# Optimization experiments

Hardware: AMD Instinct MI355X
Metric: run time of the kernel (lower is better)

## Reference

```python
import jax, jax.numpy as jnp
import numpy as np

D_MODEL = 1024
D_INNER = 1024
N_HEADS = 16
D_HEAD = D_INNER // N_HEADS
B = 2
CUR = 1024
PREV = 1024
LN_EPS = 1e-5


def _rel_shift(x):
    # x: (b, i, j, h) -- faithful to torch: pad along i, flat-reinterpret, drop first row
    b, i, j, h = x.shape
    zp = jnp.zeros((b, 1, j, h), x.dtype)
    xp = jnp.concatenate([zp, x], axis=1).reshape(i + 1, b, j, h)
    return xp[1:].reshape(b, i, j, h)


def setup_inputs() -> dict:
    key = jax.random.key(0)
    ks = jax.random.split(key, 10)
    x = jax.random.normal(ks[0], (B, CUR, D_MODEL), jnp.float32)
    mem = jax.random.normal(ks[1], (B, PREV, D_MODEL), jnp.float32)
    pos_emb = jax.random.normal(ks[2], (CUR + PREV, D_INNER), jnp.float32)
    u = jax.random.normal(ks[3], (N_HEADS, D_HEAD), jnp.float32) * 0.02
    v = jax.random.normal(ks[4], (N_HEADS, D_HEAD), jnp.float32) * 0.02
    # causal mask: query i (current segment) may attend key j if j <= i + PREV
    idx_i = jnp.arange(CUR)[:, None]
    idx_j = jnp.arange(CUR + PREV)[None, :]
    tgt_mask = jnp.broadcast_to((idx_j > idx_i + PREV)[None, :, :, None], (B, CUR, CUR + PREV, 1))
    Wq = jax.random.normal(ks[5], (D_INNER, D_MODEL), jnp.float32) * 0.02
    Wkv = jax.random.normal(ks[6], (2 * D_INNER, D_MODEL), jnp.float32) * 0.02
    Wfc = jax.random.normal(ks[7], (D_MODEL, D_INNER), jnp.float32) * 0.02
    bfc = jnp.zeros((D_MODEL,), jnp.float32)
    gamma = jnp.ones((D_MODEL,), jnp.float32)
    beta = jnp.zeros((D_MODEL,), jnp.float32)
    return {"x": x, "pos_emb": pos_emb, "u": u, "v": v, "mem": mem,
            "tgt_mask": tgt_mask, "Wq": Wq, "Wkv": Wkv, "Wfc": Wfc,
            "bfc": bfc, "gamma": gamma, "beta": beta}


def reference(x, pos_emb, u, v, mem, tgt_mask, Wq, Wkv, Wfc, bfc, gamma, beta):
    b, cur, _ = x.shape
    prev = mem.shape[1]
    tot = cur + prev
    h_telda = jnp.concatenate([mem, x], axis=1)               # (b, tot, d_model)
    q = jnp.einsum('bsm,im->bsi', x, Wq)                      # (b, cur, d_inner)
    kv = jnp.einsum('bsm,im->bsi', h_telda, Wkv)              # (b, tot, 2*d_inner)
    k, vv = kv[..., :D_INNER], kv[..., D_INNER:]
    q = q.reshape(b, cur, N_HEADS, D_HEAD)
    k = k.reshape(b, tot, N_HEADS, D_HEAD)
    vv = vv.reshape(b, tot, N_HEADS, D_HEAD)
    content = jnp.einsum('bihd,bjhd->bijh', q + u, k)
    pos = pos_emb.reshape(tot, N_HEADS, D_HEAD)
    pos_attn = jnp.einsum('bihd,jhd->bijh', q + v, pos)
    attn = content + _rel_shift(pos_attn)
    attn = jnp.where(tgt_mask, -jnp.inf, attn)
    attn = attn / (D_HEAD ** 0.5)
    attn = jax.nn.softmax(attn, axis=1)  # faithful: softmax over query dim as in original
    out = jnp.einsum('bijh,bjhd->bihd', attn, vv).reshape(b, cur, D_INNER)
    y = x + jnp.einsum('bsi,mi->bsm', out, Wfc) + bfc
    mu = jnp.mean(y, axis=-1, keepdims=True)
    var = jnp.mean((y - mu) ** 2, axis=-1, keepdims=True)
    return (y - mu) / jnp.sqrt(var + LN_EPS) * gamma + beta
```

## Files before the change

kernel.cpp:

```cpp
#include <hip/hip_runtime.h>
#include <hip/hip_bf16.h>
#include <stdint.h>

typedef unsigned short u16;
typedef __attribute__((ext_vector_type(8))) __bf16 bf16x8;
typedef __attribute__((ext_vector_type(4))) float f32x4;
typedef __attribute__((ext_vector_type(4))) float float4v;
typedef __attribute__((ext_vector_type(4))) u16  u16x4;

#define DEV __device__ __forceinline__

#define NB   2
#define CUR  1024
#define PREV 1024
#define TOT  2048
#define DM   1024
#define NH   16
#define DH   64

DEV u16 f2b(float f) {
    uint32_t u = __builtin_bit_cast(uint32_t, f);
    uint32_t r = (u + 0x7fffu + ((u >> 16) & 1u)) >> 16;
    return (u16)r;
}
DEV float b2f(u16 u) {
    return __builtin_bit_cast(float, (uint32_t)u << 16);
}

typedef const __attribute__((address_space(1))) void* gptr_t;
typedef __attribute__((address_space(3))) void*       lptr_t;
DEV void async16(const void* g, void* l) {
    __builtin_amdgcn_global_load_lds((gptr_t)g, (lptr_t)l, 16, 0, 0);
}

template<int BM, int BN, int BK, int WM, int WN, int EPI>
__global__ __launch_bounds__(256)
void gemm_bt(const u16* __restrict__ A, const u16* __restrict__ B,
             int M, int N, int K, long sA, long sB, int bzBase,
             void* __restrict__ C0, void* __restrict__ C1,
             const float* __restrict__ F0, const float* __restrict__ F1)
{
    constexpr int WAVES_N = BN / WN;
    constexpr int MI = WM / 16, NI = WN / 16;
    static_assert((BM / WM) * (BN / WN) == 4, "4 waves");
    static_assert(BK == 64, "swizzle assumes 8 chunks/row");
    static_assert((BM * BK) % 2048 == 0 && (BN * BK) % 2048 == 0, "staging");

    __shared__ u16 lA[BM * BK];
    __shared__ u16 lB[BN * BK];

    const int bz = blockIdx.z;
    const int m0 = blockIdx.y * BM, n0 = blockIdx.x * BN;
    const int tid = threadIdx.x, wave = tid >> 6, lane = tid & 63;

    if constexpr (EPI == 3) {
        if (m0 > n0 + BN - 1 + PREV) return;
    }

    const u16* Ab = A + (long)bz * sA;
    const u16* Bb = B + (long)bz * sB;
    const int wm0 = (wave / WAVES_N) * WM, wn0 = (wave % WAVES_N) * WN;
    const int quad = lane >> 4;

    f32x4 acc[MI][NI];
#pragma unroll
    for (int mi = 0; mi < MI; ++mi)
#pragma unroll
        for (int ni = 0; ni < NI; ++ni)
            acc[mi][ni] = f32x4{0.f, 0.f, 0.f, 0.f};

    int Kend = K;
    if constexpr (EPI == 4) {
        int t = n0 + BN + PREV;
        Kend = t < K ? t : K;
    }

    const int srow = tid >> 3;
    const int ksw  = (((tid & 7) ^ ((tid >> 3) & 7)) << 3);

    for (int kt = 0; kt < Kend; kt += BK) {
        __syncthreads();
#pragma unroll
        for (int is = 0; is < (BM * BK) / 2048; ++is) {
            int r = is * 32 + srow;
            async16(Ab + (long)(m0 + r) * K + kt + ksw, &lA[is * 2048 + wave * 512]);
        }
#pragma unroll
        for (int is = 0; is < (BN * BK) / 2048; ++is) {
            int r = is * 32 + srow;
            async16(Bb + (long)(n0 + r) * K + kt + ksw, &lB[is * 2048 + wave * 512]);
        }
        __syncthreads();
#pragma unroll
        for (int ks = 0; ks < BK; ks += 32) {
            bf16x8 af[MI], br[NI];
#pragma unroll
            for (int mi = 0; mi < MI; ++mi)
                af[mi] = *(const bf16x8*)(const void*)
                    &lA[(wm0 + mi * 16 + (lane & 15)) * BK +
                        ((((ks >> 3) + quad) ^ (lane & 7)) << 3)];
#pragma unroll
            for (int ni = 0; ni < NI; ++ni)
                br[ni] = *(const bf16x8*)(const void*)
                    &lB[(wn0 + ni * 16 + (lane & 15)) * BK +
                        ((((ks >> 3) + quad) ^ (lane & 7)) << 3)];
#pragma unroll
            for (int mi = 0; mi < MI; ++mi)
#pragma unroll
                for (int ni = 0; ni < NI; ++ni)
                    acc[mi][ni] = __builtin_amdgcn_mfma_f32_16x16x32_bf16(af[mi], br[ni], acc[mi][ni], 0, 0, 0);
        }
    }

    const int gbz = bzBase + bz;

    if constexpr (EPI == 1) {
        u16* Abuf = (u16*)C0;
        const int b = gbz;
#pragma unroll
        for (int mi = 0; mi < MI; ++mi) {
            const int m = m0 + wm0 + mi * 16 + quad * 4;
            const int h = m >> 6, d = m & 63;
            const float4v uu = *(const float4v*)(F0 + m);
            const float4v vv = *(const float4v*)(F1 + m);
#pragma unroll
            for (int ni = 0; ni < NI; ++ni) {
                const int i = n0 + wn0 + ni * 16 + (lane & 15);
                u16x4 pu, pv;
#pragma unroll
                for (int r = 0; r < 4; ++r) {
                    pu[r] = f2b(acc[mi][ni][r] + uu[r]);
                    pv[r] = f2b(acc[mi][ni][r] + vv[r]);
                }
                *(u16x4*)(Abuf + (((long)(b * NH + h)) * CUR + i) * 128 + d) = pu;
                if (b == 0) {
                    if (i > 0)
                        *(u16x4*)(Abuf + (((long)h) * CUR + (i - 1)) * 128 + 64 + d) = pv;
                    if (i == 1023) {
                        u16x4 z = {};
                        *(u16x4*)(Abuf + (((long)h) * CUR + 1023) * 128 + 64 + d) = z;
                    }
                } else {
                    *(u16x4*)(Abuf + (((long)(NH + h)) * CUR + i) * 128 + 64 + d) = pv;
                }
            }
        }
    } else if constexpr (EPI == 2) {
#pragma unroll
        for (int mi = 0; mi < MI; ++mi) {
            const int m = m0 + wm0 + mi * 16 + quad * 4;
            const bool isV = m >= DM;
            const int h = (m >> 6) & 15, d = m & 63;
#pragma unroll
            for (int ni = 0; ni < NI; ++ni) {
                const int n = n0 + wn0 + ni * 16 + (lane & 15);
                const int b = n >> 11, j = n & 2047;
                u16x4 p;
#pragma unroll
                for (int r = 0; r < 4; ++r) p[r] = f2b(acc[mi][ni][r]);
                if (!isV)
                    *(u16x4*)((u16*)C0 + (((long)(b * NH + h)) * TOT + j) * 128 + d) = p;
                else
                    *(u16x4*)((u16*)C1 + (((long)(b * NH + h)) * TOT + j) * 64 + d) = p;
            }
        }
    } else if constexpr (EPI == 3) {
        u16* Eb = (u16*)C0 + (long)gbz * ((long)CUR * TOT);
        float ps[MI][4];
#pragma unroll
        for (int mi = 0; mi < MI; ++mi)
#pragma unroll
            for (int r = 0; r < 4; ++r) ps[mi][r] = 0.f;
#pragma unroll
        for (int mi = 0; mi < MI; ++mi) {
            const int m = m0 + wm0 + mi * 16 + quad * 4;
#pragma unroll
            for (int ni = 0; ni < NI; ++ni) {
                const int n = n0 + wn0 + ni * 16 + (lane & 15);
                u16x4 p;
#pragma unroll
                for (int r = 0; r < 4; ++r) {
                    float e = (m + r > n + PREV) ? 0.f : __expf(acc[mi][ni][r] * 0.125f);
                    p[r] = f2b(e);
                    ps[mi][r] += e;
                }
                *(u16x4*)(Eb + (long)n * TOT + m) = p;
            }
        }
        float* CS = (float*)C1 + (long)gbz * TOT;
#pragma unroll
        for (int mi = 0; mi < MI; ++mi)
#pragma unroll
            for (int r = 0; r < 4; ++r) {
                float vv = ps[mi][r];
                vv += __shfl_xor(vv, 1);
                vv += __shfl_xor(vv, 2);
                vv += __shfl_xor(vv, 4);
                vv += __shfl_xor(vv, 8);
                if ((lane & 15) == 0)
                    atomicAdd(CS + m0 + wm0 + mi * 16 + quad * 4 + r, vv);
            }
    } else if constexpr (EPI == 4) {
        const int b = gbz >> 4, h = gbz & 15;
        u16* Ob = (u16*)C0 + (long)b * CUR * DM + h * DH;
#pragma unroll
        for (int mi = 0; mi < MI; ++mi) {
            const int m = m0 + wm0 + mi * 16 + quad * 4;
#pragma unroll
            for (int ni = 0; ni < NI; ++ni) {
                const int n = n0 + wn0 + ni * 16 + (lane & 15);
                u16x4 p;
#pragma unroll
                for (int r = 0; r < 4; ++r) p[r] = f2b(acc[mi][ni][r]);
                *(u16x4*)(Ob + (long)n * DM + m) = p;
            }
        }
    } else if constexpr (EPI == 5) {
#pragma unroll
        for (int mi = 0; mi < MI; ++mi) {
            const int m = m0 + wm0 + mi * 16 + quad * 4;
            const float4v bb = *(const float4v*)(F1 + m);
#pragma unroll
            for (int ni = 0; ni < NI; ++ni) {
                const int n = n0 + wn0 + ni * 16 + (lane & 15);
                const float4v xr = *(const float4v*)(F0 + (long)n * DM + m);
                float4v y;
#pragma unroll
                for (int r = 0; r < 4; ++r) y[r] = xr[r] + acc[mi][ni][r] + bb[r];
                *(float4v*)((float*)C0 + (long)n * DM + m) = y;
            }
        }
    }
}

__global__ __launch_bounds__(256)
void cvt_weights(const float* __restrict__ Wq, const float* __restrict__ Wkv,
                 const float* __restrict__ Wfc, u16* __restrict__ Wqb,
                 u16* __restrict__ Wkvb, u16* __restrict__ Wfcb)
{
    int i = blockIdx.x * 256 + threadIdx.x;
    const float* s; u16* d; int off;
    if (i < 262144)      { s = Wq;  d = Wqb;  off = i; }
    else if (i < 786432) { s = Wkv; d = Wkvb; off = i - 262144; }
    else                 { s = Wfc; d = Wfcb; off = i - 786432; }
    float4v f = ((const float4v*)s)[off];
    u16x4 o = {f2b(f[0]), f2b(f[1]), f2b(f[2]), f2b(f[3])};
    ((u16x4*)d)[off] = o;
}

__global__ __launch_bounds__(256)
void pack_H(const float* __restrict__ mem, const float* __restrict__ x, u16* __restrict__ dst)
{
    int i = blockIdx.x * 256 + threadIdx.x;
    int e = i << 2;
    int b = e >> 21, r = e & ((1 << 21) - 1);
    const float* src = (r < (1 << 20)) ? (mem + ((long)b << 20) + r)
                                       : (x + ((long)b << 20) + (r - (1 << 20)));
    float4v f = *(const float4v*)src;
    u16x4 o = {f2b(f[0]), f2b(f[1]), f2b(f[2]), f2b(f[3])};
    ((u16x4*)dst)[i] = o;
}

__global__ __launch_bounds__(256)
void pack_pos(const float* __restrict__ pos, u16* __restrict__ Bbuf)
{
    int i = blockIdx.x * 256 + threadIdx.x;
    int e = i << 2;
    int h = e >> 17, r = e & 131071, j = r >> 6, d = r & 63;
    float4v f = *(const float4v*)(pos + (long)j * DM + h * DH + d);
    u16x4 o = {f2b(f[0]), f2b(f[1]), f2b(f[2]), f2b(f[3])};
    long base = ((long)h * TOT + j) * 128 + 64 + d;
    *(u16x4*)(Bbuf + base) = o;
    *(u16x4*)(Bbuf + base + (long)NH * TOT * 128) = o;
}

__global__ __launch_bounds__(256)
void vprime_kernel(const u16* __restrict__ Vtmp, const float* __restrict__ colsum,
                   u16* __restrict__ Vp, int bzBase)
{
    __shared__ float t[64][65];
    int bz = bzBase + blockIdx.y;
    int j0 = blockIdx.x * 64;
    const u16* src = Vtmp + ((long)bz * TOT + j0) * 64;
    const float* cs = colsum + (long)bz * TOT + j0;
    for (int e = threadIdx.x; e < 4096; e += 256) {
        int jl = e >> 6, d = e & 63;
        t[jl][d] = b2f(src[e]) / cs[jl];
    }
    __syncthreads();
    u16* dst = Vp + (long)bz * DH * TOT + j0;
    for (int e = threadIdx.x; e < 4096; e += 256) {
        int d = e >> 6, jl = e & 63;
        dst[(long)d * TOT + jl] = f2b(t[jl][d]);
    }
}

__global__ __launch_bounds__(256)
void ln_kernel(const float* __restrict__ Y, const float* __restrict__ gamma,
               const float* __restrict__ beta, float* __restrict__ out)
{
    const int row = blockIdx.x;
    const float* y = Y + (long)row * DM;
    float v[4];
    float s = 0.f;
#pragma unroll
    for (int t = 0; t < 4; ++t) { v[t] = y[threadIdx.x + t * 256]; s += v[t]; }
#pragma unroll
    for (int off = 32; off > 0; off >>= 1) s += __shfl_down(s, off);
    __shared__ float r1[4], r2[4];
    int wv = threadIdx.x >> 6, ln = threadIdx.x & 63;
    if (ln == 0) r1[wv] = s;
    __syncthreads();
    float mu = (r1[0] + r1[1] + r1[2] + r1[3]) * (1.f / DM);
    float q = 0.f;
#pragma unroll
    for (int t = 0; t < 4; ++t) { float d = v[t] - mu; q += d * d; }
#pragma unroll
    for (int off = 32; off > 0; off >>= 1) q += __shfl_down(q, off);
    if (ln == 0) r2[wv] = q;
    __syncthreads();
    float var = (r2[0] + r2[1] + r2[2] + r2[3]) * (1.f / DM);
    float inv = rsqrtf(var + 1e-5f);
#pragma unroll
    for (int t = 0; t < 4; ++t) {
        int c = threadIdx.x + t * 256;
        out[(long)row * DM + c] = (v[t] - mu) * inv * gamma[c] + beta[c];
    }
}

extern "C" void kernel_launch(void* const* d_in, const int* in_sizes, int n_in,
                              void* d_out, int out_size, void* d_ws, size_t ws_size,
                              hipStream_t stream)
{
    const float* x     = (const float*)d_in[0];
    const float* pos   = (const float*)d_in[1];
    const float* u     = (const float*)d_in[2];
    const float* vbias = (const float*)d_in[3];
    const float* mem   = (const float*)d_in[4];
    const float* Wq    = (const float*)d_in[6];
    const float* Wkv   = (const float*)d_in[7];
    const float* Wfc   = (const float*)d_in[8];
    const float* bfc   = (const float*)d_in[9];
    const float* gamma = (const float*)d_in[10];
    const float* beta  = (const float*)d_in[11];
    float* out = (float*)d_out;

    char* w = (char*)d_ws;
    auto alloc = [&](size_t bytes) {
        char* p = w;
        w += (bytes + 255) & ~(size_t)255;
        return p;
    };
    u16*   Hb     = (u16*)alloc(4096UL * 1024 * 2);
    u16*   Wqb    = (u16*)alloc(1024UL * 1024 * 2);
    u16*   Wkvb   = (u16*)alloc(2048UL * 1024 * 2);
    u16*   Wfcb   = (u16*)alloc(1024UL * 1024 * 2);
    u16*   Abuf   = (u16*)alloc(32UL * 1024 * 128 * 2);
    u16*   Bbuf   = (u16*)alloc(32UL * 2048 * 128 * 2);
    u16*   Vtmp   = (u16*)alloc(32UL * 2048 * 64 * 2);
    u16*   Vp     = (u16*)alloc(32UL * 64 * 2048 * 2);
    float* colsum = (float*)alloc(32UL * 2048 * 4);
    u16*   Obf    = (u16*)alloc(2048UL * 1024 * 2);
    float* Yf     = (float*)alloc(2048UL * 1024 * 4);
    u16*   Ebuf   = (u16*)alloc(32UL * 1024 * 2048 * 2);

    hipMemsetAsync(colsum, 0, 32UL * 2048 * 4, stream);

    cvt_weights<<<4096, 256, 0, stream>>>(Wq, Wkv, Wfc, Wqb, Wkvb, Wfcb);
    pack_H  <<<4096, 256, 0, stream>>>(mem, x, Hb);
    pack_pos<<<2048, 256, 0, stream>>>(pos, Bbuf);

    gemm_bt<128, 64, 64, 64, 32, 1><<<dim3(16, 8, 2), 256, 0, stream>>>(
        Wqb, Hb + 1024UL * 1024, 1024, 1024, 1024, 0, 2048L * 1024, 0,
        Abuf, nullptr, u, vbias);
    gemm_bt<128, 128, 64, 64, 64, 2><<<dim3(32, 16, 1), 256, 0, stream>>>(
        Wkvb, Hb, 2048, 4096, 1024, 0, 0, 0, Bbuf, Vtmp, nullptr, nullptr);

    gemm_bt<128, 128, 64, 64, 64, 3><<<dim3(8, 16, 32), 256, 0, stream>>>(
        Bbuf, Abuf, 2048, 1024, 128, 2048L * 128, 1024L * 128, 0,
        Ebuf, colsum, nullptr, nullptr);
    vprime_kernel<<<dim3(32, 32), 256, 0, stream>>>(Vtmp, colsum, Vp, 0);
    gemm_bt<64, 64, 64, 32, 32, 4><<<dim3(16, 1, 32), 256, 0, stream>>>(
        Vp, Ebuf, 64, 1024, 2048, 64L * 2048, 1024L * 2048, 0,
        Obf, nullptr, nullptr, nullptr);

    gemm_bt<64, 128, 64, 32, 64, 5><<<dim3(16, 16, 1), 256, 0, stream>>>(
        Wfcb, Obf, 1024, 2048, 1024, 0, 0, 0, Yf, nullptr, x, bfc);
    ln_kernel<<<2048, 256, 0, stream>>>(Yf, gamma, beta, out);
}
```

Before: 185.2 us.

## Fuse score recompute, column normalization and PV into a flash-style attention kernel

Stops writing the full bf16 exp-score matrix to global memory. The column-sum pass now only accumulates exp sums, and vprime emits reciprocal column sums. A new fused kernel recomputes QK scores per 64-key tile, applies the mask, exp and reciprocal-colsum scaling, and multiplies by V through LDS. This removes a large intermediate write and read (32×1024×2048 bf16) at the cost of computing the QK^T product twice. The new kernel also runs with low parallelism (512 blocks) and uses no pipelining between tile loads and MFMA.

```diff
diff --git a/kernel.cpp b/kernel.cpp
--- a/kernel.cpp
+++ b/kernel.cpp
@@ -44,7 +44,6 @@
     constexpr int MI = WM / 16, NI = WN / 16;
     static_assert((BM / WM) * (BN / WN) == 4, "4 waves");
     static_assert(BK == 64, "swizzle assumes 8 chunks/row");
-    static_assert((BM * BK) % 2048 == 0 && (BN * BK) % 2048 == 0, "staging");
 
     __shared__ u16 lA[BM * BK];
     __shared__ u16 lB[BN * BK];
@@ -69,16 +68,10 @@
         for (int ni = 0; ni < NI; ++ni)
             acc[mi][ni] = f32x4{0.f, 0.f, 0.f, 0.f};
 
-    int Kend = K;
-    if constexpr (EPI == 4) {
-        int t = n0 + BN + PREV;
-        Kend = t < K ? t : K;
-    }
-
     const int srow = tid >> 3;
     const int ksw  = (((tid & 7) ^ ((tid >> 3) & 7)) << 3);
 
-    for (int kt = 0; kt < Kend; kt += BK) {
+    for (int kt = 0; kt < K; kt += BK) {
         __syncthreads();
 #pragma unroll
         for (int is = 0; is < (BM * BK) / 2048; ++is) {
@@ -165,7 +158,6 @@
             }
         }
     } else if constexpr (EPI == 3) {
-        u16* Eb = (u16*)C0 + (long)gbz * ((long)CUR * TOT);
         float ps[MI][4];
 #pragma unroll
         for (int mi = 0; mi < MI; ++mi)
@@ -177,14 +169,11 @@
 #pragma unroll
             for (int ni = 0; ni < NI; ++ni) {
                 const int n = n0 + wn0 + ni * 16 + (lane & 15);
-                u16x4 p;
 #pragma unroll
                 for (int r = 0; r < 4; ++r) {
                     float e = (m + r > n + PREV) ? 0.f : __expf(acc[mi][ni][r] * 0.125f);
-                    p[r] = f2b(e);
                     ps[mi][r] += e;
                 }
-                *(u16x4*)(Eb + (long)n * TOT + m) = p;
             }
         }
         float* CS = (float*)C1 + (long)gbz * TOT;
@@ -200,21 +189,6 @@
                 if ((lane & 15) == 0)
                     atomicAdd(CS + m0 + wm0 + mi * 16 + quad * 4 + r, vv);
             }
-    } else if constexpr (EPI == 4) {
-        const int b = gbz >> 4, h = gbz & 15;
-        u16* Ob = (u16*)C0 + (long)b * CUR * DM + h * DH;
-#pragma unroll
-        for (int mi = 0; mi < MI; ++mi) {
-            const int m = m0 + wm0 + mi * 16 + quad * 4;
-#pragma unroll
-            for (int ni = 0; ni < NI; ++ni) {
-                const int n = n0 + wn0 + ni * 16 + (lane & 15);
-                u16x4 p;
-#pragma unroll
-                for (int r = 0; r < 4; ++r) p[r] = f2b(acc[mi][ni][r]);
-                *(u16x4*)(Ob + (long)n * DM + m) = p;
-            }
-        }
     } else if constexpr (EPI == 5) {
 #pragma unroll
         for (int mi = 0; mi < MI; ++mi) {
@@ -230,6 +204,120 @@
                 *(float4v*)((float*)C0 + (long)n * DM + m) = y;
             }
         }
+    }
+}
+
+__global__ __launch_bounds__(256)
+void fused_attn(const u16* __restrict__ Abuf, const u16* __restrict__ Bbuf,
+                const u16* __restrict__ Vp, const float* __restrict__ rcs,
+                u16* __restrict__ Obf)
+{
+    __shared__ u16 lQ[64 * 128];
+    __shared__ u16 lK[64 * 128];
+    __shared__ u16 lV[64 * 64];
+    __shared__ u16 lP[64 * 64];
+
+    const int bh = blockIdx.y;
+    const int n0 = blockIdx.x * 64;
+    const int b = bh >> 4, h = bh & 15;
+    const int tid = threadIdx.x, wave = tid >> 6, lane = tid & 63;
+    const int l15 = lane & 15, quad = lane >> 4;
+    const int iw = wave * 16 + l15;
+
+    const u16*  Qg = Abuf + ((long)bh * CUR + n0) * 128;
+    const u16*  Kg = Bbuf + (long)bh * TOT * 128;
+    const u16*  Vg = Vp + (long)bh * DH * TOT;
+    const float* rc = rcs + (long)bh * TOT;
+
+    {
+        const int r = tid >> 4, c = tid & 15;
+        const int cs = (c & 8) | ((c & 7) ^ (r & 7));
+#pragma unroll
+        for (int is = 0; is < 4; ++is)
+            async16(Qg + (long)(is * 16 + r) * 128 + cs * 8, &lQ[is * 2048 + wave * 512]);
+    }
+
+    f32x4 oacc[4];
+#pragma unroll
+    for (int mi = 0; mi < 4; ++mi) oacc[mi] = f32x4{0.f, 0.f, 0.f, 0.f};
+
+    const int ig = n0 + iw;
+    const int nt = (n0 >> 6) + 17;
+
+    for (int t = 0; t < nt; ++t) {
+        const int j0 = t * 64;
+        __syncthreads();
+        {
+            const int r = tid >> 4, c = tid & 15;
+            const int cs = (c & 8) | ((c & 7) ^ (r & 7));
+#pragma unroll
+            for (int is = 0; is < 4; ++is)
+                async16(Kg + (long)(j0 + is * 16 + r) * 128 + cs * 8, &lK[is * 2048 + wave * 512]);
+        }
+        {
+            const int r = tid >> 3, c = tid & 7;
+            const int cs = c ^ (r & 7);
+#pragma unroll
+            for (int is = 0; is < 2; ++is)
+                async16(Vg + (long)(is * 32 + r) * TOT + j0 + cs * 8, &lV[is * 2048 + wave * 512]);
+        }
+        __syncthreads();
+
+        f32x4 sacc[4];
+#pragma unroll
+        for (int smi = 0; smi < 4; ++smi) sacc[smi] = f32x4{0.f, 0.f, 0.f, 0.f};
+#pragma unroll
+        for (int ks = 0; ks < 128; ks += 32) {
+            const int cq = (ks >> 3) + quad;
+            const bf16x8 qf = *(const bf16x8*)(const void*)
+                &lQ[iw * 128 + (((cq & 8) | ((cq & 7) ^ (iw & 7))) << 3)];
+#pragma unroll
+            for (int smi = 0; smi < 4; ++smi) {
+                const int jr = smi * 16 + l15;
+                const bf16x8 kf = *(const bf16x8*)(const void*)
+                    &lK[jr * 128 + (((cq & 8) | ((cq & 7) ^ (jr & 7))) << 3)];
+                sacc[smi] = __builtin_amdgcn_mfma_f32_16x16x32_bf16(kf, qf, sacc[smi], 0, 0, 0);
+            }
+        }
+
+#pragma unroll
+        for (int smi = 0; smi < 4; ++smi) {
+            const int jl = smi * 16 + quad * 4;
+            const int jg = j0 + jl;
+            const float4v rcv = *(const float4v*)(rc + jg);
+            u16x4 pk;
+#pragma unroll
+            for (int r = 0; r < 4; ++r) {
+                float p = (jg + r > ig + PREV) ? 0.f : __expf(sacc[smi][r] * 0.125f) * rcv[r];
+                pk[r] = f2b(p);
+            }
+            const int c16 = (jl >> 3) ^ (iw & 7);
+            *(u16x4*)&lP[iw * 64 + (c16 << 3) + ((quad & 1) << 2)] = pk;
+        }
+
+#pragma unroll
+        for (int ks = 0; ks < 64; ks += 32) {
+            const int cp = (ks >> 3) + quad;
+            const bf16x8 pb = *(const bf16x8*)(const void*)
+                &lP[iw * 64 + ((cp ^ (iw & 7)) << 3)];
+#pragma unroll
+            for (int mi = 0; mi < 4; ++mi) {
+                const int dr = mi * 16 + l15;
+                const bf16x8 vf = *(const bf16x8*)(const void*)
+                    &lV[dr * 64 + ((cp ^ (dr & 7)) << 3)];
+                oacc[mi] = __builtin_amdgcn_mfma_f32_16x16x32_bf16(vf, pb, oacc[mi], 0, 0, 0);
+            }
+        }
+    }
+
+    u16* Ob = Obf + (long)b * CUR * DM + h * DH;
+#pragma unroll
+    for (int mi = 0; mi < 4; ++mi) {
+        const int d = mi * 16 + quad * 4;
+        u16x4 p;
+#pragma unroll
+        for (int r = 0; r < 4; ++r) p[r] = f2b(oacc[mi][r]);
+        *(u16x4*)(Ob + (long)ig * DM + d) = p;
     }
 }
 
@@ -276,17 +364,19 @@
 
 __global__ __launch_bounds__(256)
 void vprime_kernel(const u16* __restrict__ Vtmp, const float* __restrict__ colsum,
-                   u16* __restrict__ Vp, int bzBase)
+                   u16* __restrict__ Vp, float* __restrict__ rcs)
 {
     __shared__ float t[64][65];
-    int bz = bzBase + blockIdx.y;
+    int bz = blockIdx.y;
     int j0 = blockIdx.x * 64;
     const u16* src = Vtmp + ((long)bz * TOT + j0) * 64;
     const float* cs = colsum + (long)bz * TOT + j0;
     for (int e = threadIdx.x; e < 4096; e += 256) {
         int jl = e >> 6, d = e & 63;
-        t[jl][d] = b2f(src[e]) / cs[jl];
-    }
+        t[jl][d] = b2f(src[e]);
+    }
+    if (threadIdx.x < 64)
+        rcs[(long)bz * TOT + j0 + threadIdx.x] = 1.f / cs[threadIdx.x];
     __syncthreads();
     u16* dst = Vp + (long)bz * DH * TOT + j0;
     for (int e = threadIdx.x; e < 4096; e += 256) {
@@ -360,9 +450,9 @@
     u16*   Vtmp   = (u16*)alloc(32UL * 2048 * 64 * 2);
     u16*   Vp     = (u16*)alloc(32UL * 64 * 2048 * 2);
     float* colsum = (float*)alloc(32UL * 2048 * 4);
+    float* rcs    = (float*)alloc(32UL * 2048 * 4);
     u16*   Obf    = (u16*)alloc(2048UL * 1024 * 2);
     float* Yf     = (float*)alloc(2048UL * 1024 * 4);
-    u16*   Ebuf   = (u16*)alloc(32UL * 1024 * 2048 * 2);
 
     hipMemsetAsync(colsum, 0, 32UL * 2048 * 4, stream);
 
@@ -378,11 +468,9 @@
 
     gemm_bt<128, 128, 64, 64, 64, 3><<<dim3(8, 16, 32), 256, 0, stream>>>(
         Bbuf, Abuf, 2048, 1024, 128, 2048L * 128, 1024L * 128, 0,
-        Ebuf, colsum, nullptr, nullptr);
-    vprime_kernel<<<dim3(32, 32), 256, 0, stream>>>(Vtmp, colsum, Vp, 0);
-    gemm_bt<64, 64, 64, 32, 32, 4><<<dim3(16, 1, 32), 256, 0, stream>>>(
-        Vp, Ebuf, 64, 1024, 2048, 64L * 2048, 1024L * 2048, 0,
-        Obf, nullptr, nullptr, nullptr);
+        nullptr, colsum, nullptr, nullptr);
+    vprime_kernel<<<dim3(32, 32), 256, 0, stream>>>(Vtmp, colsum, Vp, rcs);
+    fused_attn<<<dim3(16, 32), 256, 0, stream>>>(Abuf, Bbuf, Vp, rcs, Obf);
 
     gemm_bt<64, 128, 64, 32, 64, 5><<<dim3(16, 16, 1), 256, 0, stream>>>(
         Wfcb, Obf, 1024, 2048, 1024, 0, 0, 0, Yf, nullptr, x, bfc);
```

Result: slower. 215.1 us (+16.2%).
